# Performance work log

Hardware: AMD Instinct MI355X
Metric: run time of the kernel (lower is better)

Reference implementation:

```python
import jax, jax.numpy as jnp
import numpy as np

B, P = 8, 1000          # batch_size, num_prots
N = B * P               # total PPI nodes
E = 512000              # edges (avg degree 64)
F_HPO = 1024            # HPO feature dim (num_features)
F_MOLP = 8192           # protein molecular feature dim (hardcoded)
F_MOLD = 1024           # drug molecular feature dim (hardcoded)
D = 200
EPS = 1e-8              # torch CosineSimilarity default eps


def leaky(x):
    return jax.nn.leaky_relu(x, 0.2)


def gcn_improved(x, W, b, src, dst):
    # PyG GCNConv(improved=True): A_hat = A + 2*I, symmetrically normalized.
    h = x @ W                                                   # [N,200]
    deg = jnp.zeros((x.shape[0],), x.dtype).at[dst].add(1.0) + 2.0
    dinv = jax.lax.rsqrt(deg)
    norm = dinv[src] * dinv[dst]                                # [E]
    out = jnp.zeros_like(h).at[dst].add(norm[:, None] * h[src])  # gather->scale->scatter
    out = out + (2.0 * dinv * dinv)[:, None] * h                # self loops with weight 2
    return out + b


def setup_inputs() -> dict:
    key = jax.random.key(0)
    ks = jax.random.split(key, 30)
    def W(i, shape):
        return jax.random.normal(ks[i], shape, jnp.float32) * (1.0 / float(np.sqrt(shape[0])))
    def bvec(i, n):
        return jax.random.normal(ks[i], (n,), jnp.float32) * 0.01
    return {
        # forward inputs
        'PPI_x': jax.random.normal(ks[0], (N, F_HPO), jnp.float32),
        'protein_mol_feature': jax.random.normal(ks[1], (N, F_MOLP), jnp.float32),
        'drug_feature': jax.random.normal(ks[2], (B, F_HPO), jnp.float32),
        'drug_mol_feature': jax.random.normal(ks[3], (B, F_MOLD), jnp.float32),
        'edge_index': jax.random.randint(ks[4], (2, E), 0, N, dtype=jnp.int32),
        # frozen HPO model heads (assumed Linear -> 200)
        'hpo_drug_W': W(5, (F_HPO, D)), 'hpo_drug_b': bvec(6, D),
        'hpo_prot_W': W(7, (F_HPO, D)), 'hpo_prot_b': bvec(8, D),
        # mol_protein_model: 8192 -> 256 -> 200
        'mp_W1': W(9, (F_MOLP, 256)), 'mp_b1': bvec(10, 256),
        'mp_W2': W(11, (256, D)), 'mp_b2': bvec(12, D),
        # mol_drug_model: 1024 -> 256 -> 200
        'md_W1': W(13, (F_MOLD, 256)), 'md_b1': bvec(14, 256),
        'md_W2': W(15, (256, D)), 'md_b2': bvec(16, D),
        # fusion linears
        'pl1_W': W(17, (2 * D, D)), 'pl1_b': bvec(18, D),
        'dl1_W': W(19, (2 * D, D)), 'dl1_b': bvec(20, D),
        'dl2_W': W(21, (D, D)), 'dl2_b': bvec(22, D),
        # GCN layers
        'g1_W': W(23, (D, D)), 'g1_b': bvec(24, D),
        'g2_W': W(25, (D, D)), 'g2_b': bvec(26, D),
    }


def reference(PPI_x, protein_mol_feature, drug_feature, drug_mol_feature, edge_index,
              hpo_drug_W, hpo_drug_b, hpo_prot_W, hpo_prot_b,
              mp_W1, mp_b1, mp_W2, mp_b2, md_W1, md_b1, md_W2, md_b2,
              pl1_W, pl1_b, dl1_W, dl1_b, dl2_W, dl2_b,
              g1_W, g1_b, g2_W, g2_b):
    src, dst = edge_index[0], edge_index[1]
    # protein branch (dropout is identity in eval)
    px = PPI_x @ hpo_prot_W + hpo_prot_b                                 # [N,200]
    pm = leaky(protein_mol_feature @ mp_W1 + mp_b1) @ mp_W2 + mp_b2      # [N,200]
    px = leaky(jnp.concatenate([px, pm], axis=1))                        # [N,400]
    px = px @ pl1_W + pl1_b                                              # [N,200]
    # drug branch
    df = drug_feature @ hpo_drug_W + hpo_drug_b                          # [B,200]
    dm = leaky(drug_mol_feature @ md_W1 + md_b1) @ md_W2 + md_b2         # [B,200]
    d = leaky(jnp.concatenate([dm, df], axis=1))                         # [B,400]
    d = leaky(d @ dl1_W + dl1_b)                                         # [B,200]
    d = d @ dl2_W + dl2_b                                                # [B,200]
    d = jnp.repeat(d, P, axis=0)                                         # [B*P,200]
    # two stacked GCN layers (no nonlinearity between, as in source)
    px = gcn_improved(px, g1_W, g1_b, src, dst)
    px = gcn_improved(px, g2_W, g2_b, src, dst)
    # per-row cosine similarity (torch.nn.CosineSimilarity(dim=1))
    num = jnp.sum(d * px, axis=1)
    den = jnp.maximum(jnp.linalg.norm(d, axis=1), EPS) * jnp.maximum(jnp.linalg.norm(px, axis=1), EPS)
    sim = num / den
    return jax.nn.sigmoid(sim.reshape(B, P))
```

## Files before the change

kernel.cpp:

```cpp
#include <hip/hip_runtime.h>
#include <cstdint>
#include <cstddef>

typedef uint16_t u16;
typedef __bf16 bf16x8 __attribute__((ext_vector_type(8)));
typedef short  s16x8  __attribute__((ext_vector_type(8)));
typedef float  f32x4  __attribute__((ext_vector_type(4)));

__device__ __forceinline__ u16 f2b(float f) {
    union { float f; uint32_t u; } v; v.f = f;
    uint32_t u = v.u;
    uint32_t r = (u + 0x7FFFu + ((u >> 16) & 1u)) >> 16;
    return (u16)r;
}
__device__ __forceinline__ float b2f(u16 h) {
    union { uint32_t u; float f; } v; v.u = ((uint32_t)h) << 16;
    return v.f;
}
__device__ __forceinline__ float leakyf(float x) { return x > 0.f ? x : 0.2f * x; }
__device__ __forceinline__ void unp4(uint2 u, float& f0, float& f1, float& f2, float& f3) {
    union { uint32_t u; float f; } t;
    t.u = u.x << 16;          f0 = t.f;
    t.u = u.x & 0xffff0000u;  f1 = t.f;
    t.u = u.y << 16;          f2 = t.f;
    t.u = u.y & 0xffff0000u;  f3 = t.f;
}

static constexpr int NN = 8000;
static constexpr int EE = 512000;
static constexpr int BB = 8;

__global__ void conv_wT(const float* __restrict__ W, int Wn, int rows, int rowOff,
                        u16* __restrict__ Bt, int Kpad, int kOff, int kSpan) {
    __shared__ u16 tile[64][65];
    const int kb = blockIdx.x * 64, nb = blockIdx.y * 64;
    const int tid = threadIdx.x;
    const int ln = tid & 63, lw = tid >> 6;
    #pragma unroll
    for (int r = 0; r < 16; r++) {
        int kk = kb + lw * 16 + r;
        int n  = nb + ln;
        float v = (kk < rows && n < Wn) ? W[(size_t)(rowOff + kk) * Wn + n] : 0.f;
        tile[ln][lw * 16 + r] = f2b(v);
    }
    __syncthreads();
    #pragma unroll
    for (int r = 0; r < 16; r++) {
        int nl = lw * 16 + r;
        int kk = kb + ln;
        if (kk < kSpan) Bt[(size_t)(nb + nl) * Kpad + kOff + kk] = tile[nl][ln];
    }
}

__global__ void conv_wT5(const float* W_mp2, const float* W_pl1, const float* W_g1, const float* W_g2,
                         u16* Btmp2, u16* Btpl1, u16* Btg1, u16* Btg2) {
    __shared__ u16 tile[64][65];
    const float* W; int Wn, rows, rowOff; u16* Bt; int Kpad, kOff, kSpan;
    switch (blockIdx.z) {
        case 0: W = W_mp2; Wn = 200; rows = 256; rowOff = 0;   Bt = Btmp2; Kpad = 256; kOff = 0;   kSpan = 256; break;
        case 1: W = W_pl1; Wn = 200; rows = 200; rowOff = 0;   Bt = Btpl1; Kpad = 512; kOff = 0;   kSpan = 256; break;
        case 2: W = W_pl1; Wn = 200; rows = 200; rowOff = 200; Bt = Btpl1; Kpad = 512; kOff = 256; kSpan = 256; break;
        case 3: W = W_g1;  Wn = 200; rows = 200; rowOff = 0;   Bt = Btg1;  Kpad = 256; kOff = 0;   kSpan = 256; break;
        default:W = W_g2;  Wn = 200; rows = 200; rowOff = 0;   Bt = Btg2;  Kpad = 256; kOff = 0;   kSpan = 256; break;
    }
    const int kb = blockIdx.x * 64, nb = blockIdx.y * 64;
    const int tid = threadIdx.x;
    const int ln = tid & 63, lw = tid >> 6;
    #pragma unroll
    for (int r = 0; r < 16; r++) {
        int kk = kb + lw * 16 + r;
        int n  = nb + ln;
        float v = (kk < rows && n < Wn) ? W[(size_t)(rowOff + kk) * Wn + n] : 0.f;
        tile[ln][lw * 16 + r] = f2b(v);
    }
    __syncthreads();
    #pragma unroll
    for (int r = 0; r < 16; r++) {
        int nl = lw * 16 + r;
        int kk = kb + ln;
        if (kk < kSpan) Bt[(size_t)(nb + nl) * Kpad + kOff + kk] = tile[nl][ln];
    }
}

__global__ void padvec5(const float* p0, int n0, float* d0,
                        const float* p1, int n1, float* d1,
                        const float* p2, int n2, float* d2,
                        const float* p3, int n3, float* d3,
                        const float* p4, int n4, float* d4) {
    const float* p; int n; float* d;
    switch (blockIdx.x) {
        case 0: p = p0; n = n0; d = d0; break;
        case 1: p = p1; n = n1; d = d1; break;
        case 2: p = p2; n = n2; d = d2; break;
        case 3: p = p3; n = n3; d = d3; break;
        default: p = p4; n = n4; d = d4; break;
    }
    int i = threadIdx.x;
    d[i] = (p != nullptr && i < n) ? p[i] : 0.f;
}

__global__ void zero_i32(int* __restrict__ p, int n) {
    int i = blockIdx.x * 256 + threadIdx.x;
    if (i < n) p[i] = 0;
}

__global__ __launch_bounds__(256) void gemm_kernel(
    const void* __restrict__ Ap, int a_is_f32, int lda,
    const u16* __restrict__ Bt, int K, int kLen,
    const float* __restrict__ bias,
    void* __restrict__ Cp, int cmode, int ldc, int do_leaky, size_t partStride) {
    __shared__ u16 As[32][72];
    __shared__ u16 Bs[256][72];
    const int tid  = threadIdx.x;
    const int m0   = blockIdx.x * 32;
    const int kStart = blockIdx.y * kLen;
    const int wave = tid >> 6, lane = tid & 63;
    const int q = lane >> 4, r = lane & 15;
    const int wn = wave * 64;
    const int arow = tid & 31, akoff = (tid >> 5) * 8;
    const int brow = tid >> 2, bkoff = (tid & 3) * 16;

    f32x4 acc[2][4];
    #pragma unroll
    for (int i = 0; i < 2; i++)
        #pragma unroll
        for (int j = 0; j < 4; j++) acc[i][j] = (f32x4){0, 0, 0, 0};

    for (int k0 = kStart; k0 < kStart + kLen; k0 += 64) {
        if (a_is_f32) {
            const float* A = (const float*)Ap + (size_t)(m0 + arow) * lda + k0 + akoff;
            float fa[8];
            *(float4*)(&fa[0]) = *(const float4*)(A + 0);
            *(float4*)(&fa[4]) = *(const float4*)(A + 4);
            u16 ha[8];
            #pragma unroll
            for (int j = 0; j < 8; j++) ha[j] = f2b(fa[j]);
            *(uint4*)(&As[arow][akoff]) = *(uint4*)(&ha[0]);
        } else {
            const u16* A = (const u16*)Ap + (size_t)(m0 + arow) * lda + k0 + akoff;
            *(uint4*)(&As[arow][akoff]) = *(const uint4*)A;
        }
        #pragma unroll
        for (int p = 0; p < 4; p++) {
            const int row = p * 64 + brow;
            const u16* bp = Bt + (size_t)row * K + k0 + bkoff;
            uint4 u0 = *(const uint4*)(bp + 0);
            uint4 u1 = *(const uint4*)(bp + 8);
            *(uint4*)(&Bs[row][bkoff])     = u0;
            *(uint4*)(&Bs[row][bkoff + 8]) = u1;
        }
        __syncthreads();
        #pragma unroll
        for (int ks = 0; ks < 2; ks++) {
            const int kb = ks * 32 + q * 8;
            s16x8 a0 = *(const s16x8*)(&As[r][kb]);
            s16x8 a1 = *(const s16x8*)(&As[16 + r][kb]);
            s16x8 b0 = *(const s16x8*)(&Bs[wn +      r][kb]);
            s16x8 b1 = *(const s16x8*)(&Bs[wn + 16 + r][kb]);
            s16x8 b2 = *(const s16x8*)(&Bs[wn + 32 + r][kb]);
            s16x8 b3 = *(const s16x8*)(&Bs[wn + 48 + r][kb]);
            acc[0][0] = __builtin_amdgcn_mfma_f32_16x16x32_bf16(__builtin_bit_cast(bf16x8, a0), __builtin_bit_cast(bf16x8, b0), acc[0][0], 0, 0, 0);
            acc[0][1] = __builtin_amdgcn_mfma_f32_16x16x32_bf16(__builtin_bit_cast(bf16x8, a0), __builtin_bit_cast(bf16x8, b1), acc[0][1], 0, 0, 0);
            acc[0][2] = __builtin_amdgcn_mfma_f32_16x16x32_bf16(__builtin_bit_cast(bf16x8, a0), __builtin_bit_cast(bf16x8, b2), acc[0][2], 0, 0, 0);
            acc[0][3] = __builtin_amdgcn_mfma_f32_16x16x32_bf16(__builtin_bit_cast(bf16x8, a0), __builtin_bit_cast(bf16x8, b3), acc[0][3], 0, 0, 0);
            acc[1][0] = __builtin_amdgcn_mfma_f32_16x16x32_bf16(__builtin_bit_cast(bf16x8, a1), __builtin_bit_cast(bf16x8, b0), acc[1][0], 0, 0, 0);
            acc[1][1] = __builtin_amdgcn_mfma_f32_16x16x32_bf16(__builtin_bit_cast(bf16x8, a1), __builtin_bit_cast(bf16x8, b1), acc[1][1], 0, 0, 0);
            acc[1][2] = __builtin_amdgcn_mfma_f32_16x16x32_bf16(__builtin_bit_cast(bf16x8, a1), __builtin_bit_cast(bf16x8, b2), acc[1][2], 0, 0, 0);
            acc[1][3] = __builtin_amdgcn_mfma_f32_16x16x32_bf16(__builtin_bit_cast(bf16x8, a1), __builtin_bit_cast(bf16x8, b3), acc[1][3], 0, 0, 0);
        }
        __syncthreads();
    }

    #pragma unroll
    for (int ti = 0; ti < 2; ti++)
        #pragma unroll
        for (int tj = 0; tj < 4; tj++)
            #pragma unroll
            for (int reg = 0; reg < 4; reg++) {
                int gr = m0 + ti * 16 + q * 4 + reg;
                int gc = wn + tj * 16 + r;
                float v = acc[ti][tj][reg];
                if (cmode == 2) {
                    ((float*)Cp)[blockIdx.y * partStride + (size_t)gr * 256 + gc] = v;
                } else {
                    v += bias[gc];
                    if (do_leaky) v = leakyf(v);
                    if (cmode == 1) ((u16*)Cp)[(size_t)gr * ldc + gc] = f2b(v);
                    else            ((float*)Cp)[(size_t)gr * ldc + gc] = v;
                }
            }
}

__global__ void reduce_k(const float* __restrict__ part, size_t partStride, int S,
                         const float* __restrict__ bias, void* __restrict__ out,
                         int out_bf16, int ldc, int do_leaky) {
    int i = blockIdx.x * 256 + threadIdx.x;
    float v = 0.f;
    for (int s = 0; s < S; s++) v += part[s * partStride + i];
    int col = i & 255, row = i >> 8;
    v += bias[col];
    if (do_leaky) v = leakyf(v);
    if (out_bf16) ((u16*)out)[(size_t)row * ldc + col] = f2b(v);
    else          ((float*)out)[(size_t)row * ldc + col] = v;
}

__global__ void count_kernel(const int* __restrict__ dst, int* __restrict__ cnt) {
    int e = blockIdx.x * 256 + threadIdx.x;
    if (e < EE) atomicAdd(&cnt[dst[e]], 1);
}
__global__ void scan_kernel(const int* __restrict__ cnt, int* __restrict__ row_start,
                            int* __restrict__ cursor, float* __restrict__ dinv) {
    __shared__ int part[1024];
    const int tid = threadIdx.x;
    int local[8];
    int s = 0;
    const int base = tid * 8;
    #pragma unroll
    for (int j = 0; j < 8; j++) { int idx = base + j; int v = (idx < NN) ? cnt[idx] : 0; local[j] = s; s += v; }
    part[tid] = s;
    __syncthreads();
    for (int off = 1; off < 1024; off <<= 1) {
        int v = (tid >= off) ? part[tid - off] : 0;
        __syncthreads();
        part[tid] += v;
        __syncthreads();
    }
    const int excl = (tid == 0) ? 0 : part[tid - 1];
    #pragma unroll
    for (int j = 0; j < 8; j++) {
        int idx = base + j;
        if (idx < NN) {
            int v = excl + local[j];
            row_start[idx] = v; cursor[idx] = v;
            dinv[idx] = rsqrtf((float)cnt[idx] + 2.0f);
        }
    }
    if (tid == 1023) row_start[NN] = part[1023];
}
__global__ void fill_kernel(const int* __restrict__ src, const int* __restrict__ dst,
                            int* __restrict__ cursor, const float* __restrict__ dinv,
                            int* __restrict__ csr_src, float* __restrict__ csr_w) {
    int e = blockIdx.x * 256 + threadIdx.x;
    if (e < EE) {
        int s = src[e], d = dst[e];
        int pos = atomicAdd(&cursor[d], 1);
        csr_src[pos] = s;
        csr_w[pos]   = dinv[s] * dinv[d];
    }
}

__global__ __launch_bounds__(256) void agg_kernel(
    const u16* __restrict__ h, const float* __restrict__ dinv,
    const int* __restrict__ row_start, const int* __restrict__ csr_src,
    const float* __restrict__ csr_w, const float* __restrict__ bias,
    u16* __restrict__ out_bf16, const float* __restrict__ dhat,
    float* __restrict__ out_sig) {
    const int wave = threadIdx.x >> 6, lane = threadIdx.x & 63;
    const int node = blockIdx.x * 4 + wave;
    const int start = row_start[node], end = row_start[node + 1];
    const float di = dinv[node];

    float a0, a1, a2, a3;
    {
        uint2 hv = *(const uint2*)(h + (size_t)node * 256 + lane * 4);
        float f0, f1, f2, f3; unp4(hv, f0, f1, f2, f3);
        float sl = 2.f * di * di;
        a0 = sl * f0; a1 = sl * f1; a2 = sl * f2; a3 = sl * f3;
    }

    for (int p = start; p < end; p += 64) {
        const int n = min(64, end - p);
        int   mySrc = 0;
        float myW   = 0.f;
        if (lane < n) { mySrc = csr_src[p + lane]; myW = csr_w[p + lane]; }
        int j0 = 0;
        for (; j0 + 8 <= n; j0 += 8) {
            int sj[8]; float wj[8]; uint2 rj[8];
            #pragma unroll
            for (int j = 0; j < 8; j++) { sj[j] = __shfl(mySrc, j0 + j); wj[j] = __shfl(myW, j0 + j); }
            #pragma unroll
            for (int j = 0; j < 8; j++) rj[j] = *(const uint2*)(h + (size_t)sj[j] * 256 + lane * 4);
            #pragma unroll
            for (int j = 0; j < 8; j++) {
                float f0, f1, f2, f3; unp4(rj[j], f0, f1, f2, f3);
                a0 += wj[j] * f0; a1 += wj[j] * f1; a2 += wj[j] * f2; a3 += wj[j] * f3;
            }
        }
        for (; j0 < n; j0++) {
            int s = __shfl(mySrc, j0);
            float w = __shfl(myW, j0);
            uint2 rv = *(const uint2*)(h + (size_t)s * 256 + lane * 4);
            float f0, f1, f2, f3; unp4(rv, f0, f1, f2, f3);
            a0 += w * f0; a1 += w * f1; a2 += w * f2; a3 += w * f3;
        }
    }

    if (out_bf16 != nullptr) {
        uint2 o = {0u, 0u};
        if (lane < 50) {
            float4 bv = *(const float4*)(bias + lane * 4);
            u16 h0 = f2b(a0 + bv.x), h1 = f2b(a1 + bv.y), h2 = f2b(a2 + bv.z), h3 = f2b(a3 + bv.w);
            o.x = (uint32_t)h0 | ((uint32_t)h1 << 16);
            o.y = (uint32_t)h2 | ((uint32_t)h3 << 16);
        }
        *(uint2*)(out_bf16 + (size_t)node * 256 + lane * 4) = o;
    } else {
        float dot = 0.f, nn2 = 0.f;
        if (lane < 50) {
            float4 bv = *(const float4*)(bias + lane * 4);
            float4 dv = *(const float4*)(dhat + (node / 1000) * 200 + lane * 4);
            float v0 = a0 + bv.x, v1 = a1 + bv.y, v2 = a2 + bv.z, v3 = a3 + bv.w;
            dot = v0 * dv.x + v1 * dv.y + v2 * dv.z + v3 * dv.w;
            nn2 = v0 * v0 + v1 * v1 + v2 * v2 + v3 * v3;
        }
        #pragma unroll
        for (int off = 32; off; off >>= 1) {
            dot += __shfl_xor(dot, off, 64);
            nn2 += __shfl_xor(nn2, off, 64);
        }
        if (lane == 0) {
            float sim = dot / fmaxf(sqrtf(nn2), 1e-8f);
            out_sig[node] = 1.f / (1.f + expf(-sim));
        }
    }
}

__global__ void drug_kernel(const float* __restrict__ drugF, const float* __restrict__ drugM,
                            const float* __restrict__ hW, const float* __restrict__ hb,
                            const float* __restrict__ m1W, const float* __restrict__ m1b,
                            const float* __restrict__ m2W, const float* __restrict__ m2b,
                            const float* __restrict__ l1W, const float* __restrict__ l1b,
                            const float* __restrict__ l2W, const float* __restrict__ l2b,
                            float* __restrict__ dhat) {
    const int b = blockIdx.x, tid = threadIdx.x;
    __shared__ float sF[1024], sM[1024], sT[256], s400[400], s200[200], sred[256];
    for (int k = tid; k < 1024; k += 256) { sF[k] = drugF[b * 1024 + k]; sM[k] = drugM[b * 1024 + k]; }
    __syncthreads();
    {
        float acc = m1b[tid];
        for (int k = 0; k < 1024; k++) acc += sM[k] * m1W[k * 256 + tid];
        sT[tid] = leakyf(acc);
    }
    float dfv = 0.f;
    if (tid < 200) {
        dfv = hb[tid];
        for (int k = 0; k < 1024; k++) dfv += sF[k] * hW[k * 200 + tid];
    }
    __syncthreads();
    if (tid < 200) {
        float acc = m2b[tid];
        for (int k = 0; k < 256; k++) acc += sT[k] * m2W[k * 200 + tid];
        s400[tid]       = leakyf(acc);
        s400[200 + tid] = leakyf(dfv);
    }
    __syncthreads();
    if (tid < 200) {
        float acc = l1b[tid];
        for (int k = 0; k < 400; k++) acc += s400[k] * l1W[k * 200 + tid];
        s200[tid] = leakyf(acc);
    }
    __syncthreads();
    float dv = 0.f;
    if (tid < 200) {
        dv = l2b[tid];
        for (int k = 0; k < 200; k++) dv += s200[k] * l2W[k * 200 + tid];
    }
    sred[tid] = (tid < 200) ? dv * dv : 0.f;
    __syncthreads();
    for (int off = 128; off; off >>= 1) {
        if (tid < off) sred[tid] += sred[tid + off];
        __syncthreads();
    }
    float nrm = fmaxf(sqrtf(sred[0]), 1e-8f);
    if (tid < 200) dhat[b * 200 + tid] = dv / nrm;
}

extern "C" void kernel_launch(void* const* d_in, const int* in_sizes, int n_in,
                              void* d_out, int out_size, void* d_ws, size_t ws_size,
                              hipStream_t stream) {
    const float* PPI_x = (const float*)d_in[0];
    const float* PMF   = (const float*)d_in[1];
    const float* drugF = (const float*)d_in[2];
    const float* drugM = (const float*)d_in[3];
    const int*   eidx  = (const int*)d_in[4];
    const float* hpo_drug_W = (const float*)d_in[5];
    const float* hpo_drug_b = (const float*)d_in[6];
    const float* hpo_prot_W = (const float*)d_in[7];
    const float* hpo_prot_b = (const float*)d_in[8];
    const float* mp_W1 = (const float*)d_in[9];
    const float* mp_b1 = (const float*)d_in[10];
    const float* mp_W2 = (const float*)d_in[11];
    const float* mp_b2 = (const float*)d_in[12];
    const float* md_W1 = (const float*)d_in[13];
    const float* md_b1 = (const float*)d_in[14];
    const float* md_W2 = (const float*)d_in[15];
    const float* md_b2 = (const float*)d_in[16];
    const float* pl1_W = (const float*)d_in[17];
    const float* pl1_b = (const float*)d_in[18];
    const float* dl1_W = (const float*)d_in[19];
    const float* dl1_b = (const float*)d_in[20];
    const float* dl2_W = (const float*)d_in[21];
    const float* dl2_b = (const float*)d_in[22];
    const float* g1_W  = (const float*)d_in[23];
    const float* g1_b  = (const float*)d_in[24];
    const float* g2_W  = (const float*)d_in[25];
    const float* g2_b  = (const float*)d_in[26];

    char* wsp = (char*)d_ws;
    size_t off = 0;
    auto alloc = [&](size_t bytes) -> void* {
        size_t o = (off + 255) & ~(size_t)255;
        off = o + bytes;
        return (void*)(wsp + o);
    };

    u16* cb    = (u16*)alloc((size_t)NN * 512 * 2);
    u16* t1    = (u16*)alloc((size_t)NN * 256 * 2);
    u16* px2   = (u16*)alloc((size_t)NN * 256 * 2);
    u16* hbuf  = (u16*)alloc((size_t)NN * 256 * 2);
    float* part = (float*)alloc((size_t)4 * NN * 256 * 4);
    u16* Btmp1 = (u16*)alloc((size_t)256 * 8192 * 2);
    u16* Bthpo = (u16*)alloc((size_t)256 * 1024 * 2);
    u16* Btmp2 = (u16*)alloc((size_t)256 * 256 * 2);
    u16* Btpl1 = (u16*)alloc((size_t)256 * 512 * 2);
    u16* Btg1  = (u16*)alloc((size_t)256 * 256 * 2);
    u16* Btg2  = (u16*)alloc((size_t)256 * 256 * 2);
    float* bias_hpo = (float*)alloc(256 * 4);
    float* bias_m1  = (float*)alloc(256 * 4);
    float* bias_m2  = (float*)alloc(256 * 4);
    float* bias_pl  = (float*)alloc(256 * 4);
    float* zero256  = (float*)alloc(256 * 4);
    float* dhat     = (float*)alloc((size_t)BB * 200 * 4);
    int*   deg      = (int*)alloc((size_t)NN * 4);
    float* dinv     = (float*)alloc((size_t)NN * 4);
    int*   row_st   = (int*)alloc((size_t)(NN + 4) * 4);
    int*   cursor   = (int*)alloc((size_t)NN * 4);
    int*   csr_src  = (int*)alloc((size_t)EE * 4);
    float* csr_w    = (float*)alloc((size_t)EE * 4);

    u16* y1 = t1;
    const size_t PSTRIDE = (size_t)NN * 256;

    const int* e_src = eidx;
    const int* e_dst = eidx + EE;

    conv_wT<<<dim3(16, 4),  256, 0, stream>>>(hpo_prot_W, 200, 1024, 0, Bthpo, 1024, 0, 1024);
    conv_wT<<<dim3(128, 4), 256, 0, stream>>>(mp_W1,      256, 8192, 0, Btmp1, 8192, 0, 8192);
    conv_wT5<<<dim3(4, 4, 5), 256, 0, stream>>>(mp_W2, pl1_W, g1_W, g2_W, Btmp2, Btpl1, Btg1, Btg2);
    padvec5<<<5, 256, 0, stream>>>(hpo_prot_b, 200, bias_hpo,
                                   mp_b1,      256, bias_m1,
                                   mp_b2,      200, bias_m2,
                                   pl1_b,      200, bias_pl,
                                   nullptr,    0,   zero256);

    drug_kernel<<<BB, 256, 0, stream>>>(drugF, drugM, hpo_drug_W, hpo_drug_b,
                                        md_W1, md_b1, md_W2, md_b2,
                                        dl1_W, dl1_b, dl2_W, dl2_b, dhat);

    const int MB = NN / 32;
    const int RG = (NN * 256) / 256;

    gemm_kernel<<<dim3(MB, 4), 256, 0, stream>>>(PPI_x, 1, 1024, Bthpo, 1024, 256, zero256, part, 2, 256, 0, PSTRIDE);
    reduce_k<<<RG, 256, 0, stream>>>(part, PSTRIDE, 4, bias_hpo, cb, 1, 512, 1);
    gemm_kernel<<<dim3(MB, 4), 256, 0, stream>>>(PMF, 1, 8192, Btmp1, 8192, 2048, zero256, part, 2, 256, 0, PSTRIDE);
    reduce_k<<<RG, 256, 0, stream>>>(part, PSTRIDE, 4, bias_m1, t1, 1, 256, 1);
    gemm_kernel<<<dim3(MB, 1), 256, 0, stream>>>(t1, 0, 256, Btmp2, 256, 256, bias_m2, cb + 256, 1, 512, 1, 0);
    gemm_kernel<<<dim3(MB, 1), 256, 0, stream>>>(cb, 0, 512, Btpl1, 512, 512, bias_pl, px2, 1, 256, 0, 0);

    zero_i32<<<(NN + 255) / 256, 256, 0, stream>>>(deg, NN);
    count_kernel<<<EE / 256, 256, 0, stream>>>(e_dst, deg);
    scan_kernel<<<1, 1024, 0, stream>>>(deg, row_st, cursor, dinv);
    fill_kernel<<<EE / 256, 256, 0, stream>>>(e_src, e_dst, cursor, dinv, csr_src, csr_w);

    gemm_kernel<<<dim3(MB, 1), 256, 0, stream>>>(px2, 0, 256, Btg1, 256, 256, zero256, hbuf, 1, 256, 0, 0);
    agg_kernel<<<NN / 4, 256, 0, stream>>>(hbuf, dinv, row_st, csr_src, csr_w, g1_b, y1, nullptr, nullptr);
    gemm_kernel<<<dim3(MB, 1), 256, 0, stream>>>(y1, 0, 256, Btg2, 256, 256, zero256, hbuf, 1, 256, 0, 0);
    agg_kernel<<<NN / 4, 256, 0, stream>>>(hbuf, dinv, row_st, csr_src, csr_w, g2_b, nullptr, dhat, (float*)d_out);
}
```

Before: 889.3 us.

## Double-buffer GEMM tiles with async global-to-LDS loads and reduce split-K

```diff
diff --git a/kernel.cpp b/kernel.cpp
--- a/kernel.cpp
+++ b/kernel.cpp
@@ -29,6 +29,10 @@
 static constexpr int NN = 8000;
 static constexpr int EE = 512000;
 static constexpr int BB = 8;
+
+#define GLOAD_LDS16(gp, lp)                                                              \
+    __builtin_amdgcn_global_load_lds((const __attribute__((address_space(1))) void*)(gp), \
+                                     (__attribute__((address_space(3))) void*)(lp), 16, 0, 0)
 
 __global__ void conv_wT(const float* __restrict__ W, int Wn, int rows, int rowOff,
                         u16* __restrict__ Bt, int Kpad, int kOff, int kSpan) {
@@ -109,8 +113,8 @@
     const u16* __restrict__ Bt, int K, int kLen,
     const float* __restrict__ bias,
     void* __restrict__ Cp, int cmode, int ldc, int do_leaky, size_t partStride) {
-    __shared__ u16 As[32][72];
-    __shared__ u16 Bs[256][72];
+    __shared__ u16 As[2][32][72];
+    __shared__ u16 Bs[2][16384];
     const int tid  = threadIdx.x;
     const int m0   = blockIdx.x * 32;
     const int kStart = blockIdx.y * kLen;
@@ -118,7 +122,7 @@
     const int q = lane >> 4, r = lane & 15;
     const int wn = wave * 64;
     const int arow = tid & 31, akoff = (tid >> 5) * 8;
-    const int brow = tid >> 2, bkoff = (tid & 3) * 16;
+    const int nIter = kLen >> 6;
 
     f32x4 acc[2][4];
     #pragma unroll
@@ -126,39 +130,65 @@
         #pragma unroll
         for (int j = 0; j < 4; j++) acc[i][j] = (f32x4){0, 0, 0, 0};
 
-    for (int k0 = kStart; k0 < kStart + kLen; k0 += 64) {
+    auto stageB = [&](int buf, int k0) {
+        #pragma unroll
+        for (int c = 0; c < 8; ++c) {
+            const int idx16 = c * 256 + tid;
+            const int row   = idx16 >> 3;
+            const int gs    = (idx16 & 7) ^ (row & 7);
+            const u16* src  = Bt + (size_t)row * K + k0 + gs * 8;
+            u16* dst = &Bs[buf][0] + c * 2048 + wave * 512;
+            GLOAD_LDS16(src, dst);
+        }
+    };
+    float4 fa0, fa1; uint4 ua;
+    auto loadA = [&](int k0) {
         if (a_is_f32) {
             const float* A = (const float*)Ap + (size_t)(m0 + arow) * lda + k0 + akoff;
-            float fa[8];
-            *(float4*)(&fa[0]) = *(const float4*)(A + 0);
-            *(float4*)(&fa[4]) = *(const float4*)(A + 4);
-            u16 ha[8];
-            #pragma unroll
-            for (int j = 0; j < 8; j++) ha[j] = f2b(fa[j]);
-            *(uint4*)(&As[arow][akoff]) = *(uint4*)(&ha[0]);
+            fa0 = *(const float4*)A;
+            fa1 = *(const float4*)(A + 4);
         } else {
             const u16* A = (const u16*)Ap + (size_t)(m0 + arow) * lda + k0 + akoff;
-            *(uint4*)(&As[arow][akoff]) = *(const uint4*)A;
-        }
-        #pragma unroll
-        for (int p = 0; p < 4; p++) {
-            const int row = p * 64 + brow;
-            const u16* bp = Bt + (size_t)row * K + k0 + bkoff;
-            uint4 u0 = *(const uint4*)(bp + 0);
-            uint4 u1 = *(const uint4*)(bp + 8);
-            *(uint4*)(&Bs[row][bkoff])     = u0;
-            *(uint4*)(&Bs[row][bkoff + 8]) = u1;
-        }
-        __syncthreads();
+            ua = *(const uint4*)A;
+        }
+    };
+    auto writeA = [&](int buf) {
+        uint4 w;
+        if (a_is_f32) {
+            u16 h[8];
+            h[0] = f2b(fa0.x); h[1] = f2b(fa0.y); h[2] = f2b(fa0.z); h[3] = f2b(fa0.w);
+            h[4] = f2b(fa1.x); h[5] = f2b(fa1.y); h[6] = f2b(fa1.z); h[7] = f2b(fa1.w);
+            w = *(uint4*)h;
+        } else w = ua;
+        *(uint4*)(&As[buf][arow][akoff]) = w;
+    };
+
+    loadA(kStart);
+    stageB(0, kStart);
+    writeA(0);
+    __syncthreads();
+
+    int cur = 0;
+    for (int t = 0; t < nIter; ++t) {
+        const int nb = cur ^ 1;
+        const bool hasNext = (t + 1 < nIter);
+        if (hasNext) {
+            const int k1 = kStart + (t + 1) * 64;
+            loadA(k1);
+            stageB(nb, k1);
+        }
+        const char* BsC = (const char*)&Bs[cur][0];
         #pragma unroll
         for (int ks = 0; ks < 2; ks++) {
             const int kb = ks * 32 + q * 8;
-            s16x8 a0 = *(const s16x8*)(&As[r][kb]);
-            s16x8 a1 = *(const s16x8*)(&As[16 + r][kb]);
-            s16x8 b0 = *(const s16x8*)(&Bs[wn +      r][kb]);
-            s16x8 b1 = *(const s16x8*)(&Bs[wn + 16 + r][kb]);
-            s16x8 b2 = *(const s16x8*)(&Bs[wn + 32 + r][kb]);
-            s16x8 b3 = *(const s16x8*)(&Bs[wn + 48 + r][kb]);
+            s16x8 a0 = *(const s16x8*)(&As[cur][r][kb]);
+            s16x8 a1 = *(const s16x8*)(&As[cur][16 + r][kb]);
+            const int swz  = ((ks << 2) + q) ^ (r & 7);
+            const int boff = ((wn + r) << 7) + (swz << 4);
+            s16x8 b0 = *(const s16x8*)(BsC + boff);
+            s16x8 b1 = *(const s16x8*)(BsC + boff + 2048);
+            s16x8 b2 = *(const s16x8*)(BsC + boff + 4096);
+            s16x8 b3 = *(const s16x8*)(BsC + boff + 6144);
             acc[0][0] = __builtin_amdgcn_mfma_f32_16x16x32_bf16(__builtin_bit_cast(bf16x8, a0), __builtin_bit_cast(bf16x8, b0), acc[0][0], 0, 0, 0);
             acc[0][1] = __builtin_amdgcn_mfma_f32_16x16x32_bf16(__builtin_bit_cast(bf16x8, a0), __builtin_bit_cast(bf16x8, b1), acc[0][1], 0, 0, 0);
             acc[0][2] = __builtin_amdgcn_mfma_f32_16x16x32_bf16(__builtin_bit_cast(bf16x8, a0), __builtin_bit_cast(bf16x8, b2), acc[0][2], 0, 0, 0);
@@ -168,7 +198,9 @@
             acc[1][2] = __builtin_amdgcn_mfma_f32_16x16x32_bf16(__builtin_bit_cast(bf16x8, a1), __builtin_bit_cast(bf16x8, b2), acc[1][2], 0, 0, 0);
             acc[1][3] = __builtin_amdgcn_mfma_f32_16x16x32_bf16(__builtin_bit_cast(bf16x8, a1), __builtin_bit_cast(bf16x8, b3), acc[1][3], 0, 0, 0);
         }
+        if (hasNext) writeA(nb);
         __syncthreads();
+        cur = nb;
     }
 
     #pragma unroll
@@ -418,7 +450,7 @@
     u16* t1    = (u16*)alloc((size_t)NN * 256 * 2);
     u16* px2   = (u16*)alloc((size_t)NN * 256 * 2);
     u16* hbuf  = (u16*)alloc((size_t)NN * 256 * 2);
-    float* part = (float*)alloc((size_t)4 * NN * 256 * 4);
+    float* part = (float*)alloc((size_t)2 * NN * 256 * 4);
     u16* Btmp1 = (u16*)alloc((size_t)256 * 8192 * 2);
     u16* Bthpo = (u16*)alloc((size_t)256 * 1024 * 2);
     u16* Btmp2 = (u16*)alloc((size_t)256 * 256 * 2);
@@ -460,10 +492,9 @@
     const int MB = NN / 32;
     const int RG = (NN * 256) / 256;
 
-    gemm_kernel<<<dim3(MB, 4), 256, 0, stream>>>(PPI_x, 1, 1024, Bthpo, 1024, 256, zero256, part, 2, 256, 0, PSTRIDE);
-    reduce_k<<<RG, 256, 0, stream>>>(part, PSTRIDE, 4, bias_hpo, cb, 1, 512, 1);
-    gemm_kernel<<<dim3(MB, 4), 256, 0, stream>>>(PMF, 1, 8192, Btmp1, 8192, 2048, zero256, part, 2, 256, 0, PSTRIDE);
-    reduce_k<<<RG, 256, 0, stream>>>(part, PSTRIDE, 4, bias_m1, t1, 1, 256, 1);
+    gemm_kernel<<<dim3(MB, 1), 256, 0, stream>>>(PPI_x, 1, 1024, Bthpo, 1024, 1024, bias_hpo, cb, 1, 512, 1, 0);
+    gemm_kernel<<<dim3(MB, 2), 256, 0, stream>>>(PMF, 1, 8192, Btmp1, 8192, 4096, zero256, part, 2, 256, 0, PSTRIDE);
+    reduce_k<<<RG, 256, 0, stream>>>(part, PSTRIDE, 2, bias_m1, t1, 1, 256, 1);
     gemm_kernel<<<dim3(MB, 1), 256, 0, stream>>>(t1, 0, 256, Btmp2, 256, 256, bias_m2, cb + 256, 1, 512, 1, 0);
     gemm_kernel<<<dim3(MB, 1), 256, 0, stream>>>(cb, 0, 512, Btpl1, 512, 512, bias_pl, px2, 1, 256, 0, 0);
 
```

Result: no change. 906.6 us (+1.9%).

## Use direct global-to-LDS loads with XOR swizzle and 64-row tiles for big GEMMs

Applied to the files above, without the earlier changes.

```diff
diff --git a/kernel.cpp b/kernel.cpp
--- a/kernel.cpp
+++ b/kernel.cpp
@@ -29,6 +29,10 @@
 static constexpr int NN = 8000;
 static constexpr int EE = 512000;
 static constexpr int BB = 8;
+
+#define GLOAD_LDS16(gp, lp)                                                              \
+    __builtin_amdgcn_global_load_lds((const __attribute__((address_space(1))) void*)(gp), \
+                                     (__attribute__((address_space(3))) void*)(lp), 16, 0, 0)
 
 __global__ void conv_wT(const float* __restrict__ W, int Wn, int rows, int rowOff,
                         u16* __restrict__ Bt, int Kpad, int kOff, int kSpan) {
@@ -104,75 +108,101 @@
     if (i < n) p[i] = 0;
 }
 
+template<int BM>
 __global__ __launch_bounds__(256) void gemm_kernel(
     const void* __restrict__ Ap, int a_is_f32, int lda,
     const u16* __restrict__ Bt, int K, int kLen,
     const float* __restrict__ bias,
     void* __restrict__ Cp, int cmode, int ldc, int do_leaky, size_t partStride) {
-    __shared__ u16 As[32][72];
-    __shared__ u16 Bs[256][72];
+    constexpr int MREP = BM / 16;
+    __shared__ u16 As[BM][72];
+    __shared__ u16 Bs[16384];
     const int tid  = threadIdx.x;
-    const int m0   = blockIdx.x * 32;
+    const int m0   = blockIdx.x * BM;
     const int kStart = blockIdx.y * kLen;
     const int wave = tid >> 6, lane = tid & 63;
     const int q = lane >> 4, r = lane & 15;
     const int wn = wave * 64;
-    const int arow = tid & 31, akoff = (tid >> 5) * 8;
-    const int brow = tid >> 2, bkoff = (tid & 3) * 16;
-
-    f32x4 acc[2][4];
-    #pragma unroll
-    for (int i = 0; i < 2; i++)
+
+    f32x4 acc[MREP][4];
+    #pragma unroll
+    for (int i = 0; i < MREP; i++)
         #pragma unroll
         for (int j = 0; j < 4; j++) acc[i][j] = (f32x4){0, 0, 0, 0};
 
     for (int k0 = kStart; k0 < kStart + kLen; k0 += 64) {
-        if (a_is_f32) {
-            const float* A = (const float*)Ap + (size_t)(m0 + arow) * lda + k0 + akoff;
-            float fa[8];
-            *(float4*)(&fa[0]) = *(const float4*)(A + 0);
-            *(float4*)(&fa[4]) = *(const float4*)(A + 4);
-            u16 ha[8];
-            #pragma unroll
-            for (int j = 0; j < 8; j++) ha[j] = f2b(fa[j]);
-            *(uint4*)(&As[arow][akoff]) = *(uint4*)(&ha[0]);
+        #pragma unroll
+        for (int c = 0; c < 8; ++c) {
+            const int idx16 = c * 256 + tid;
+            const int row   = idx16 >> 3;
+            const int gs    = (idx16 & 7) ^ (row & 7);
+            const u16* src  = Bt + (size_t)row * K + k0 + gs * 8;
+            u16* dst = &Bs[0] + c * 2048 + wave * 512;
+            GLOAD_LDS16(src, dst);
+        }
+        if (BM == 64) {
+            const int ar = tid >> 2, ac = (tid & 3) * 16;
+            if (a_is_f32) {
+                const float* A = (const float*)Ap + (size_t)(m0 + ar) * lda + k0 + ac;
+                float4 f0 = *(const float4*)(A + 0);
+                float4 f1 = *(const float4*)(A + 4);
+                float4 f2 = *(const float4*)(A + 8);
+                float4 f3 = *(const float4*)(A + 12);
+                u16 h[16];
+                h[0]=f2b(f0.x); h[1]=f2b(f0.y); h[2]=f2b(f0.z); h[3]=f2b(f0.w);
+                h[4]=f2b(f1.x); h[5]=f2b(f1.y); h[6]=f2b(f1.z); h[7]=f2b(f1.w);
+                h[8]=f2b(f2.x); h[9]=f2b(f2.y); h[10]=f2b(f2.z); h[11]=f2b(f2.w);
+                h[12]=f2b(f3.x); h[13]=f2b(f3.y); h[14]=f2b(f3.z); h[15]=f2b(f3.w);
+                *(uint4*)(&As[ar][ac])     = ((uint4*)h)[0];
+                *(uint4*)(&As[ar][ac + 8]) = ((uint4*)h)[1];
+            } else {
+                const u16* A = (const u16*)Ap + (size_t)(m0 + ar) * lda + k0 + ac;
+                uint4 u0 = *(const uint4*)(A + 0);
+                uint4 u1 = *(const uint4*)(A + 8);
+                *(uint4*)(&As[ar][ac])     = u0;
+                *(uint4*)(&As[ar][ac + 8]) = u1;
+            }
         } else {
-            const u16* A = (const u16*)Ap + (size_t)(m0 + arow) * lda + k0 + akoff;
-            *(uint4*)(&As[arow][akoff]) = *(const uint4*)A;
-        }
-        #pragma unroll
-        for (int p = 0; p < 4; p++) {
-            const int row = p * 64 + brow;
-            const u16* bp = Bt + (size_t)row * K + k0 + bkoff;
-            uint4 u0 = *(const uint4*)(bp + 0);
-            uint4 u1 = *(const uint4*)(bp + 8);
-            *(uint4*)(&Bs[row][bkoff])     = u0;
-            *(uint4*)(&Bs[row][bkoff + 8]) = u1;
+            const int ar = tid >> 3, ac = (tid & 7) * 8;
+            if (a_is_f32) {
+                const float* A = (const float*)Ap + (size_t)(m0 + ar) * lda + k0 + ac;
+                float4 f0 = *(const float4*)(A + 0);
+                float4 f1 = *(const float4*)(A + 4);
+                u16 h[8];
+                h[0]=f2b(f0.x); h[1]=f2b(f0.y); h[2]=f2b(f0.z); h[3]=f2b(f0.w);
+                h[4]=f2b(f1.x); h[5]=f2b(f1.y); h[6]=f2b(f1.z); h[7]=f2b(f1.w);
+                *(uint4*)(&As[ar][ac]) = *(uint4*)h;
+            } else {
+                const u16* A = (const u16*)Ap + (size_t)(m0 + ar) * lda + k0 + ac;
+                *(uint4*)(&As[ar][ac]) = *(const uint4*)A;
+            }
         }
         __syncthreads();
         #pragma unroll
         for (int ks = 0; ks < 2; ks++) {
             const int kb = ks * 32 + q * 8;
-            s16x8 a0 = *(const s16x8*)(&As[r][kb]);
-            s16x8 a1 = *(const s16x8*)(&As[16 + r][kb]);
-            s16x8 b0 = *(const s16x8*)(&Bs[wn +      r][kb]);
-            s16x8 b1 = *(const s16x8*)(&Bs[wn + 16 + r][kb]);
-            s16x8 b2 = *(const s16x8*)(&Bs[wn + 32 + r][kb]);
-            s16x8 b3 = *(const s16x8*)(&Bs[wn + 48 + r][kb]);
-            acc[0][0] = __builtin_amdgcn_mfma_f32_16x16x32_bf16(__builtin_bit_cast(bf16x8, a0), __builtin_bit_cast(bf16x8, b0), acc[0][0], 0, 0, 0);
-            acc[0][1] = __builtin_amdgcn_mfma_f32_16x16x32_bf16(__builtin_bit_cast(bf16x8, a0), __builtin_bit_cast(bf16x8, b1), acc[0][1], 0, 0, 0);
-            acc[0][2] = __builtin_amdgcn_mfma_f32_16x16x32_bf16(__builtin_bit_cast(bf16x8, a0), __builtin_bit_cast(bf16x8, b2), acc[0][2], 0, 0, 0);
-            acc[0][3] = __builtin_amdgcn_mfma_f32_16x16x32_bf16(__builtin_bit_cast(bf16x8, a0), __builtin_bit_cast(bf16x8, b3), acc[0][3], 0, 0, 0);
-            acc[1][0] = __builtin_amdgcn_mfma_f32_16x16x32_bf16(__builtin_bit_cast(bf16x8, a1), __builtin_bit_cast(bf16x8, b0), acc[1][0], 0, 0, 0);
-            acc[1][1] = __builtin_amdgcn_mfma_f32_16x16x32_bf16(__builtin_bit_cast(bf16x8, a1), __builtin_bit_cast(bf16x8, b1), acc[1][1], 0, 0, 0);
-            acc[1][2] = __builtin_amdgcn_mfma_f32_16x16x32_bf16(__builtin_bit_cast(bf16x8, a1), __builtin_bit_cast(bf16x8, b2), acc[1][2], 0, 0, 0);
-            acc[1][3] = __builtin_amdgcn_mfma_f32_16x16x32_bf16(__builtin_bit_cast(bf16x8, a1), __builtin_bit_cast(bf16x8, b3), acc[1][3], 0, 0, 0);
+            s16x8 a[MREP];
+            #pragma unroll
+            for (int m = 0; m < MREP; m++) a[m] = *(const s16x8*)(&As[m * 16 + r][kb]);
+            const int swz  = ((ks << 2) + q) ^ (r & 7);
+            const int boff = ((wn + r) << 7) + (swz << 4);
+            const char* BsC = (const char*)&Bs[0];
+            s16x8 b[4];
+            #pragma unroll
+            for (int j = 0; j < 4; j++) b[j] = *(const s16x8*)(BsC + boff + j * 2048);
+            #pragma unroll
+            for (int m = 0; m < MREP; m++)
+                #pragma unroll
+                for (int j = 0; j < 4; j++)
+                    acc[m][j] = __builtin_amdgcn_mfma_f32_16x16x32_bf16(
+                        __builtin_bit_cast(bf16x8, a[m]), __builtin_bit_cast(bf16x8, b[j]),
+                        acc[m][j], 0, 0, 0);
         }
         __syncthreads();
     }
 
     #pragma unroll
-    for (int ti = 0; ti < 2; ti++)
+    for (int ti = 0; ti < MREP; ti++)
         #pragma unroll
         for (int tj = 0; tj < 4; tj++)
             #pragma unroll
@@ -457,23 +487,22 @@
                                         md_W1, md_b1, md_W2, md_b2,
                                         dl1_W, dl1_b, dl2_W, dl2_b, dhat);
 
-    const int MB = NN / 32;
     const int RG = (NN * 256) / 256;
 
-    gemm_kernel<<<dim3(MB, 4), 256, 0, stream>>>(PPI_x, 1, 1024, Bthpo, 1024, 256, zero256, part, 2, 256, 0, PSTRIDE);
+    gemm_kernel<64><<<dim3(125, 4), 256, 0, stream>>>(PPI_x, 1, 1024, Bthpo, 1024, 256, zero256, part, 2, 256, 0, PSTRIDE);
     reduce_k<<<RG, 256, 0, stream>>>(part, PSTRIDE, 4, bias_hpo, cb, 1, 512, 1);
-    gemm_kernel<<<dim3(MB, 4), 256, 0, stream>>>(PMF, 1, 8192, Btmp1, 8192, 2048, zero256, part, 2, 256, 0, PSTRIDE);
+    gemm_kernel<64><<<dim3(125, 4), 256, 0, stream>>>(PMF, 1, 8192, Btmp1, 8192, 2048, zero256, part, 2, 256, 0, PSTRIDE);
     reduce_k<<<RG, 256, 0, stream>>>(part, PSTRIDE, 4, bias_m1, t1, 1, 256, 1);
-    gemm_kernel<<<dim3(MB, 1), 256, 0, stream>>>(t1, 0, 256, Btmp2, 256, 256, bias_m2, cb + 256, 1, 512, 1, 0);
-    gemm_kernel<<<dim3(MB, 1), 256, 0, stream>>>(cb, 0, 512, Btpl1, 512, 512, bias_pl, px2, 1, 256, 0, 0);
+    gemm_kernel<32><<<dim3(250, 1), 256, 0, stream>>>(t1, 0, 256, Btmp2, 256, 256, bias_m2, cb + 256, 1, 512, 1, 0);
+    gemm_kernel<32><<<dim3(250, 1), 256, 0, stream>>>(cb, 0, 512, Btpl1, 512, 512, bias_pl, px2, 1, 256, 0, 0);
 
     zero_i32<<<(NN + 255) / 256, 256, 0, stream>>>(deg, NN);
     count_kernel<<<EE / 256, 256, 0, stream>>>(e_dst, deg);
     scan_kernel<<<1, 1024, 0, stream>>>(deg, row_st, cursor, dinv);
     fill_kernel<<<EE / 256, 256, 0, stream>>>(e_src, e_dst, cursor, dinv, csr_src, csr_w);
 
-    gemm_kernel<<<dim3(MB, 1), 256, 0, stream>>>(px2, 0, 256, Btg1, 256, 256, zero256, hbuf, 1, 256, 0, 0);
+    gemm_kernel<32><<<dim3(250, 1), 256, 0, stream>>>(px2, 0, 256, Btg1, 256, 256, zero256, hbuf, 1, 256, 0, 0);
     agg_kernel<<<NN / 4, 256, 0, stream>>>(hbuf, dinv, row_st, csr_src, csr_w, g1_b, y1, nullptr, nullptr);
-    gemm_kernel<<<dim3(MB, 1), 256, 0, stream>>>(y1, 0, 256, Btg2, 256, 256, zero256, hbuf, 1, 256, 0, 0);
+    gemm_kernel<32><<<dim3(250, 1), 256, 0, stream>>>(y1, 0, 256, Btg2, 256, 256, zero256, hbuf, 1, 256, 0, 0);
     agg_kernel<<<NN / 4, 256, 0, stream>>>(hbuf, dinv, row_st, csr_src, csr_w, g2_b, nullptr, dhat, (float*)d_out);
 }
```

After: 822.5 us. 7.5% less time.
